# Optimization experiments

Hardware: AMD Instinct MI355X
Metric: run time of the kernel (lower is better)

## Reference

```python
import jax, jax.numpy as jnp
import numpy as np

F = 3          # features
E = 2 * F      # transformer d_model
H = F          # n_heads (head_dim = 2)
FF = 2048      # torch TransformerEncoderLayer default dim_feedforward
OUT = 4
STRIDE = 2
N_BATCH = 16
T_LEN = 2046
LN_EPS = 1e-5


def setup_inputs() -> dict:
    key = jax.random.key(0)
    ks = iter(jax.random.split(key, 48))

    def p(shape, s=0.1):
        return jax.random.normal(next(ks), shape, dtype=jnp.float32) * s

    inp = {
        "x": jax.random.normal(next(ks), (N_BATCH, T_LEN, F), dtype=jnp.float32),
        # multi-scale depthwise conv kernels/biases
        "k64": p((8, F, 64)), "b64": p((8, F)),
        "k16": p((F, 16)), "b16": p((F,)),
        "k8": p((F, 8)), "b8": p((F,)),
        # stage-2 width-3 channel convs
        "kw3": p((F, 3)), "bw3": p((F,)),
        "km3": p((F, 3)), "bm3": p((F,)),
        "kn3": p((F, 3)), "bn3": p((F,)),
        # hidden FCs
        "fc1_w": p((6 * F, 12 * F)), "fc1_b": p((6 * F,)),
        "fc2_w": p((E, 6 * F)), "fc2_b": p((E,)),
        # 2 transformer encoder layers (stacked along leading dim)
        "inw": p((2, 3 * E, E)), "inb": p((2, 3 * E)),
        "ow": p((2, E, E)), "ob": p((2, E)),
        "l1w": jnp.ones((2, E), jnp.float32), "l1b": jnp.zeros((2, E), jnp.float32),
        "l2w": jnp.ones((2, E), jnp.float32), "l2b": jnp.zeros((2, E), jnp.float32),
        "f1w": p((2, FF, E)), "f1b": p((2, FF)),
        "f2w": p((2, E, FF)), "f2b": p((2, E)),
        # output head
        "out1_w": p((7, E)), "out1_b": p((7,)),
        "out2_w": p((OUT, 7)),
    }
    return inp


def _ln(y, w, b):
    mu = y.mean(-1, keepdims=True)
    var = ((y - mu) ** 2).mean(-1, keepdims=True)
    return (y - mu) / jnp.sqrt(var + LN_EPS) * w + b


def _conv3_same(y, k, b):
    # depthwise width-3 'same' conv over seq dim; y:(N,L,F), k:(F,3), b:(F,)
    yp = jnp.pad(y, ((0, 0), (1, 1), (0, 0)))
    return k[:, 0] * yp[:, :-2] + k[:, 1] * yp[:, 1:-1] + k[:, 2] * yp[:, 2:] + b


def _forward(x, k64, b64, k16, b16, k8, b8, kw3, bw3, km3, bm3, kn3, bn3,
             fc1_w, fc1_b, fc2_w, fc2_b, inw, inb, ow, ob,
             l1w, l1b, l2w, l2b, f1w, f1b, f2w, f2b, out1_w, out1_b, out2_w):
    N, T, _ = x.shape
    PAD = 40
    px = jnp.pad(x, ((0, 0), (PAD, PAD), (0, 0)))
    W = T // STRIDE + 1
    centers = PAD + 1 + STRIDE * jnp.arange(W)  # wide window centers
    starts = centers - 32
    relu = jax.nn.relu

    # wide: 8 depthwise width-64 kernels per center -> (N, 8W, F)
    wwin = px[:, centers[:, None] + jnp.arange(-32, 32), :]        # (N,W,64,F)
    wide = jnp.einsum('nwtf,kft->nwkf', wwin, k64) + b64[None, None]
    wide = wide.reshape(N, 8 * W, F)  # center-major, kernel-minor (loop order)

    # mid: width-16 kernel at 8 centers per window -> (N, 8W, F)
    mid_c = (starts[:, None] + 8 * jnp.arange(8)).reshape(-1)
    mwin = px[:, mid_c[:, None] + jnp.arange(-8, 8), :]            # (N,8W,16,F)
    mid = jnp.einsum('nctf,ft->ncf', mwin, k16) + b16

    # narrow: width-8 kernel at 32 centers per window, then maxpool4 -> (N, 8W, F)
    nar_c = (starts[:, None] + 2 * jnp.arange(32)).reshape(-1)
    nwin = px[:, nar_c[:, None] + jnp.arange(-4, 4), :]            # (N,32W,8,F)
    nar = jnp.einsum('nctf,ft->ncf', nwin, k8) + b8
    nar = nar.reshape(N, 8 * W, 4, F).max(axis=2)

    wide = 5.0 * relu(wide)  # residual=0, dropout=0 -> drop is identity
    mid = relu(mid)
    nar = relu(nar)

    wide = relu(_conv3_same(wide, kw3, bw3))
    mid = relu(_conv3_same(mid, km3, bm3))
    nar = relu(_conv3_same(nar, kn3, bn3))

    def pool2(y):  # MaxPool1d(2) over seq dim
        return y.reshape(N, 4 * W, 2, F).max(axis=2)
    wide, mid, nar = pool2(wide), pool2(mid), pool2(nar)

    S = W  # (4W) // 4 blocks

    def blocks(y):  # (N,4W,F) -> (N,S,4F), time-major flatten per block
        return y.reshape(N, S, 4 * F)
    flat = jnp.concatenate([blocks(wide), blocks(mid), blocks(nar)], axis=-1)

    h = relu(flat @ fc1_w.T + fc1_b)  # residual=0 -> (1-residual)*h + 0
    h = relu(h @ fc2_w.T + fc2_b)     # (N,S,E)
    seq = jnp.transpose(h, (1, 0, 2))  # (S,N,E), torch seq-first layout

    d = E // H
    scale = 1.0 / jnp.sqrt(jnp.float32(d))
    for l in range(2):  # post-LN TransformerEncoder, 2 layers
        qkv = seq @ inw[l].T + inb[l]                 # (S,N,3E)
        q, k_, v = jnp.split(qkv, 3, axis=-1)
        q = q.reshape(S, N, H, d)
        k_ = k_.reshape(S, N, H, d)
        v = v.reshape(S, N, H, d)
        att = jnp.einsum('snhd,tnhd->nhst', q, k_) * scale
        p_att = jax.nn.softmax(att, axis=-1)
        o = jnp.einsum('nhst,tnhd->snhd', p_att, v).reshape(S, N, E)
        o = o @ ow[l].T + ob[l]
        seq = _ln(seq + o, l1w[l], l1b[l])
        ff = relu(seq @ f1w[l].T + f1b[l]) @ f2w[l].T + f2b[l]
        seq = _ln(seq + ff, l2w[l], l2b[l])

    pooled = relu(seq.mean(axis=0))           # AvgPool1d over full seq -> (N,E)
    o1 = relu(pooled @ out1_w.T + out1_b)
    logits = o1 @ out2_w.T                    # no bias
    return jax.nn.log_softmax(logits, axis=1)


def reference(x, k64, b64, k16, b16, k8, b8, kw3, bw3, km3, bm3, kn3, bn3,
              fc1_w, fc1_b, fc2_w, fc2_b, inw, inb, ow, ob,
              l1w, l1b, l2w, l2b, f1w, f1b, f2w, f2b, out1_w, out1_b, out2_w):
    return _forward(x, k64, b64, k16, b16, k8, b8, kw3, bw3, km3, bm3, kn3, bn3,
                    fc1_w, fc1_b, fc2_w, fc2_b, inw, inb, ow, ob,
                    l1w, l1b, l2w, l2b, f1w, f1b, f2w, f2b, out1_w, out1_b, out2_w)
```

## Files before the change

kernel.cpp:

```cpp
#include <hip/hip_runtime.h>
#include <math.h>


#define TL 2046
#define SL 1024

typedef float f32x2 __attribute__((ext_vector_type(2)));

__device__ __forceinline__ float relu_(float a){ return fmaxf(a, 0.f); }
__device__ __forceinline__ float fexp2_(float x){ return __builtin_amdgcn_exp2f(x); }
__device__ __forceinline__ float dpp_xadd1(float x){
  return x + __int_as_float(__builtin_amdgcn_update_dpp(
      0, __float_as_int(x), 0xB1, 0xF, 0xF, true));
}
__device__ __forceinline__ float dpp_xadd2(float x){
  return x + __int_as_float(__builtin_amdgcn_update_dpp(
      0, __float_as_int(x), 0x4E, 0xF, 0xF, true));
}

__device__ __forceinline__ f32x2 pk_fma_blo(f32x2 a, f32x2 b, f32x2 c){
  f32x2 d;
  asm("v_pk_fma_f32 %0, %1, %2, %3 op_sel:[0,0,0] op_sel_hi:[1,0,1]"
      : "=v"(d) : "v"(a), "v"(b), "v"(c));
  return d;
}
__device__ __forceinline__ f32x2 pk_fma_bhi(f32x2 a, f32x2 b, f32x2 c){
  f32x2 d;
  asm("v_pk_fma_f32 %0, %1, %2, %3 op_sel:[0,1,0] op_sel_hi:[1,1,1]"
      : "=v"(d) : "v"(a), "v"(b), "v"(c));
  return d;
}
__device__ __forceinline__ f32x2 pk_fma_blo_clo(f32x2 a, f32x2 b, f32x2 c){
  f32x2 d;
  asm("v_pk_fma_f32 %0, %1, %2, %3 op_sel:[0,0,0] op_sel_hi:[1,0,0]"
      : "=v"(d) : "v"(a), "v"(b), "v"(c));
  return d;
}
__device__ __forceinline__ f32x2 pk_mul_bhi(f32x2 a, f32x2 b){
  f32x2 d;
  asm("v_pk_mul_f32 %0, %1, %2 op_sel:[0,1] op_sel_hi:[1,1]"
      : "=v"(d) : "v"(a), "v"(b));
  return d;
}
__device__ __forceinline__ f32x2 pk_add2(f32x2 a, f32x2 b){
  f32x2 d;
  asm("v_pk_add_f32 %0, %1, %2" : "=v"(d) : "v"(a), "v"(b));
  return d;
}

#define SCQK 1.0201265650432017f

__global__ __launch_bounds__(192) void frontend_kernel(
  const float* __restrict__ x, const float* __restrict__ k64,
  const float* __restrict__ b64, const float* __restrict__ k16, const float* __restrict__ b16,
  const float* __restrict__ k8,  const float* __restrict__ b8,
  const float* __restrict__ kw3, const float* __restrict__ bw3,
  const float* __restrict__ km3, const float* __restrict__ bm3,
  const float* __restrict__ kn3, const float* __restrict__ bn3,
  const float* __restrict__ fc1w, const float* __restrict__ fc1b,
  const float* __restrict__ fc2w, const float* __restrict__ fc2b,
  const float* __restrict__ f1w, const float* __restrict__ f1b,
  const float* __restrict__ f2w,
  const float* __restrict__ inw, const float* __restrict__ inb,
  float* __restrict__ fcc, float* __restrict__ seq,
  float4* __restrict__ kv4, float2* __restrict__ qq)
{
  __shared__ float xt[3][200];
  __shared__ float k64s[3*64*8];
  __shared__ float flat_s[64][44];
  __shared__ float h1_s[64][20];
  __shared__ float seq6[64][6];
  const int tid  = threadIdx.x;
  const int f    = tid >> 6;
  const int lane = tid & 63;
  const int n    = blockIdx.x >> 4;
  const int s0   = (blockIdx.x & 15) << 6;
  const int s    = s0 + lane;

  for (int i = blockIdx.x*192 + tid; i < 2*2048*16; i += 256*192){
    int l = i >> 15, r = i & 32767, j = r >> 4, c = r & 15;
    float v = 0.f;
    if (c < 6)       v = f1w[(l*2048 + j)*6 + c];
    else if (c == 6) v = f1b[l*2048 + j];
    else if (c >= 8 && c < 14) v = f2w[(l*6 + (c-8))*2048 + j];
    fcc[i] = v;
  }

  for (int i = tid; i < 600; i += 192){
    int ff = i / 200, pos = i - ff*200;
    int xp = 2*s0 - 39 + pos;
    xt[ff][pos] = (xp >= 0 && xp < TL) ? x[(n*TL + xp)*3 + ff] : 0.f;
  }
  for (int i = tid; i < 1536; i += 192){
    int ff = i >> 9, r = i & 511, t = r >> 3, k = r & 7;
    k64s[i] = k64[k*192 + ff*64 + t];
  }
  __syncthreads();

  float xr[74];
  {
    const int b = 2*lane;
    #pragma unroll
    for (int i = 0; i < 74; i++) xr[i] = xt[f][b + i];
  }

  float accw[8], acc_e0, acc_e1;
  #pragma unroll
  for (int k = 0; k < 8; k++) accw[k] = b64[k*3 + f];
  acc_e0 = accw[7]; acc_e1 = accw[0];
  {
    const float* kp = &k64s[f*512];
    #pragma unroll
    for (int t = 0; t < 64; t++){
      float4 wa = *(const float4*)(kp + t*8);
      float4 wb = *(const float4*)(kp + t*8 + 4);
      float xm = xr[8 + t];
      accw[0] = fmaf(xm, wa.x, accw[0]);
      accw[1] = fmaf(xm, wa.y, accw[1]);
      accw[2] = fmaf(xm, wa.z, accw[2]);
      accw[3] = fmaf(xm, wa.w, accw[3]);
      accw[4] = fmaf(xm, wb.x, accw[4]);
      accw[5] = fmaf(xm, wb.y, accw[5]);
      accw[6] = fmaf(xm, wb.z, accw[6]);
      accw[7] = fmaf(xm, wb.w, accw[7]);
      acc_e0 = fmaf(xr[6 + t],  wb.w, acc_e0);
      acc_e1 = fmaf(xr[10 + t], wa.x, acc_e1);
    }
  }
  float yw[10];
  yw[0] = (s > 0) ? 5.f*relu_(acc_e0) : 0.f;
  #pragma unroll
  for (int c = 1; c <= 8; c++) yw[c] = 5.f*relu_(accw[c-1]);
  yw[9] = (s < 1023) ? 5.f*relu_(acc_e1) : 0.f;

  float w16r[16];
  #pragma unroll
  for (int t = 0; t < 16; t++) w16r[t] = k16[f*16 + t];
  const float bb16 = b16[f];
  float ym[10];
  #pragma unroll
  for (int ci = 0; ci < 10; ci++){
    const int b = (ci == 0) ? 54 : ((ci == 9) ? 2 : 8*(ci-1));
    float a = bb16;
    #pragma unroll
    for (int t = 0; t < 16; t++) a = fmaf(xr[b + t], w16r[t], a);
    ym[ci] = relu_(a);
  }
  if (s == 0)    ym[0] = 0.f;
  if (s == 1023) ym[9] = 0.f;

  float w8r[8];
  #pragma unroll
  for (int t = 0; t < 8; t++) w8r[t] = k8[f*8 + t];
  const float bb8 = b8[f];
  float yn[10];
  #pragma unroll
  for (int ci = 0; ci < 10; ci++){
    float m = -3.0e38f;
    #pragma unroll
    for (int j2 = 0; j2 < 4; j2++){
      const int b = (ci == 0) ? (58 + 2*j2)
                  : ((ci == 9) ? (6 + 2*j2)
                               : (4 + 2*(4*(ci-1) + j2)));
      float a = bb8;
      #pragma unroll
      for (int t = 0; t < 8; t++) a = fmaf(xr[b + t], w8r[t], a);
      m = fmaxf(m, a);
    }
    yn[ci] = relu_(m);
  }
  if (s == 0)    yn[0] = 0.f;
  if (s == 1023) yn[9] = 0.f;

  {
    float c0 = kw3[f*3], c1 = kw3[f*3+1], c2 = kw3[f*3+2], bb = bw3[f];
    #pragma unroll
    for (int q = 0; q < 4; q++){
      float z0 = relu_(fmaf(c0, yw[2*q],   fmaf(c1, yw[2*q+1], fmaf(c2, yw[2*q+2], bb))));
      float z1 = relu_(fmaf(c0, yw[2*q+1], fmaf(c1, yw[2*q+2], fmaf(c2, yw[2*q+3], bb))));
      flat_s[lane][q*3 + f] = fmaxf(z0, z1);
    }
  }
  {
    float c0 = km3[f*3], c1 = km3[f*3+1], c2 = km3[f*3+2], bb = bm3[f];
    #pragma unroll
    for (int q = 0; q < 4; q++){
      float z0 = relu_(fmaf(c0, ym[2*q],   fmaf(c1, ym[2*q+1], fmaf(c2, ym[2*q+2], bb))));
      float z1 = relu_(fmaf(c0, ym[2*q+1], fmaf(c1, ym[2*q+2], fmaf(c2, ym[2*q+3], bb))));
      flat_s[lane][12 + q*3 + f] = fmaxf(z0, z1);
    }
  }
  {
    float c0 = kn3[f*3], c1 = kn3[f*3+1], c2 = kn3[f*3+2], bb = bn3[f];
    #pragma unroll
    for (int q = 0; q < 4; q++){
      float z0 = relu_(fmaf(c0, yn[2*q],   fmaf(c1, yn[2*q+1], fmaf(c2, yn[2*q+2], bb))));
      float z1 = relu_(fmaf(c0, yn[2*q+1], fmaf(c1, yn[2*q+2], fmaf(c2, yn[2*q+3], bb))));
      flat_s[lane][24 + q*3 + f] = fmaxf(z0, z1);
    }
  }
  __syncthreads();

  #pragma unroll
  for (int oi = 0; oi < 6; oi++){
    const int o = 6*f + oi;
    float acc = fc1b[o];
    const float4* wrow = (const float4*)(fc1w + o*36);
    const float4* frow = (const float4*)(&flat_s[lane][0]);
    #pragma unroll
    for (int i = 0; i < 9; i++){
      float4 wv = wrow[i], fv = frow[i];
      acc = fmaf(wv.x, fv.x, acc); acc = fmaf(wv.y, fv.y, acc);
      acc = fmaf(wv.z, fv.z, acc); acc = fmaf(wv.w, fv.w, acc);
    }
    h1_s[lane][o] = relu_(acc);
  }
  __syncthreads();

  #pragma unroll
  for (int ei = 0; ei < 2; ei++){
    const int e = 2*f + ei;
    float acc = fc2b[e];
    #pragma unroll
    for (int o = 0; o < 18; o++) acc = fmaf(h1_s[lane][o], fc2w[e*18 + o], acc);
    float v = acc < 0.f ? 0.f : acc;
    seq[(n*SL + s)*6 + e] = v;
    seq6[lane][e] = v;
  }
  __syncthreads();

  {
    const int g = f;
    float sv[6];
    #pragma unroll
    for (int e = 0; e < 6; e++) sv[e] = seq6[lane][e];
    const int h2 = 2*g;
    float q0 = inb[h2],   q1 = inb[h2+1];
    float k0 = inb[6+h2], k1 = inb[7+h2];
    float v0 = inb[12+h2], v1 = inb[13+h2];
    #pragma unroll
    for (int e = 0; e < 6; e++){
      q0 = fmaf(sv[e], inw[h2*6 + e],      q0);
      q1 = fmaf(sv[e], inw[(h2+1)*6 + e],  q1);
      k0 = fmaf(sv[e], inw[(6+h2)*6 + e],  k0);
      k1 = fmaf(sv[e], inw[(7+h2)*6 + e],  k1);
      v0 = fmaf(sv[e], inw[(12+h2)*6 + e], v0);
      v1 = fmaf(sv[e], inw[(13+h2)*6 + e], v1);
    }
    const int nh = n*3 + g;
    kv4[nh*SL + s] = make_float4(k0*SCQK, k1*SCQK, v0, v1);
    qq [nh*SL + s] = make_float2(q0, q1);
  }
}

__global__ __launch_bounds__(512, 4) void attn_kernel(
  const float4* __restrict__ kv4, const float2* __restrict__ qq,
  float* __restrict__ att_out)
{
  __shared__ float4 sKV[1024];
  __shared__ float red[8][8][8][3];
  const int tid  = threadIdx.x;
  const int w    = tid >> 6;
  const int lane = tid & 63;
  const int rb   = blockIdx.x << 6;
  const int h    = blockIdx.y;
  const int n    = blockIdx.z;
  const int nh   = n*3 + h;

  const float4* kvp = kv4 + nh*SL;
  sKV[tid]       = kvp[tid];
  sKV[tid + 512] = kvp[tid + 512];

  const int r0 = rb + w*8;
  f32x2 q0p[4], q1p[4];
  {
    const float2* qp = qq + nh*SL + r0;
    #pragma unroll
    for (int p = 0; p < 4; p++){
      float2 qa = qp[2*p], qb = qp[2*p+1];
      q0p[p] = f32x2{qa.x, qb.x};
      q1p[p] = f32x2{qa.y, qb.y};
    }
  }
  __syncthreads();

  f32x2 lvp[4], o0p[4], o1p[4];
  #pragma unroll
  for (int p = 0; p < 4; p++){ lvp[p] = 0.f; o0p[p] = 0.f; o1p[p] = 0.f; }

  #pragma unroll 2
  for (int i = 0; i < 16; i++){
    float4 K = sKV[i*64 + lane];
    f32x2 pA = f32x2{K.x, K.y};
    f32x2 pB = f32x2{K.z, K.w};
    #pragma unroll
    for (int p = 0; p < 4; p++){
      f32x2 sc = pk_fma_blo(q0p[p], pA, pk_mul_bhi(q1p[p], pA));
      f32x2 pe;
      pe.x = fexp2_(sc.x);
      pe.y = fexp2_(sc.y);
      lvp[p] = pk_add2(lvp[p], pe);
      o0p[p] = pk_fma_blo(pe, pB, o0p[p]);
      o1p[p] = pk_fma_bhi(pe, pB, o1p[p]);
    }
  }

  float lv[8], o0[8], o1[8];
  #pragma unroll
  for (int p = 0; p < 4; p++){
    lv[2*p] = lvp[p].x;  lv[2*p+1] = lvp[p].y;
    o0[2*p] = o0p[p].x;  o0[2*p+1] = o0p[p].y;
    o1[2*p] = o1p[p].x;  o1[2*p+1] = o1p[p].y;
  }
  #pragma unroll
  for (int r = 0; r < 8; r++){
    lv[r] = dpp_xadd1(lv[r]); lv[r] = dpp_xadd2(lv[r]); lv[r] += __shfl_xor(lv[r], 4);
    o0[r] = dpp_xadd1(o0[r]); o0[r] = dpp_xadd2(o0[r]); o0[r] += __shfl_xor(o0[r], 4);
    o1[r] = dpp_xadd1(o1[r]); o1[r] = dpp_xadd2(o1[r]); o1[r] += __shfl_xor(o1[r], 4);
  }
  {
    const int g = lane >> 3;
    #pragma unroll
    for (int r = 0; r < 8; r++){
      if ((lane & 7) == r){
        red[w][g][r][0] = lv[r];
        red[w][g][r][1] = o0[r];
        red[w][g][r][2] = o1[r];
      }
    }
  }
  __syncthreads();

  if (tid < 64){
    const int ww = tid >> 3, r = tid & 7;
    float L = 0.f, O0 = 0.f, O1 = 0.f;
    #pragma unroll
    for (int g = 0; g < 8; g++){
      L  += red[ww][g][r][0];
      O0 += red[ww][g][r][1];
      O1 += red[ww][g][r][2];
    }
    const float inv = 1.0f / L;
    float* orow = att_out + (n*SL + rb + tid)*6 + 2*h;
    orow[0] = O0*inv; orow[1] = O1*inv;
  }
}

__global__ __launch_bounds__(512, 4) void ff_kernel(
  const float* __restrict__ seq_in, const float* __restrict__ att,
  const float* __restrict__ fcc,
  const float* __restrict__ ow, const float* __restrict__ ob,
  const float* __restrict__ l1w, const float* __restrict__ l1b,
  float* __restrict__ seq_mid, float* __restrict__ ffp, int layer)
{
  __shared__ float wc[512][16];
  __shared__ float sM[128][6];
  const int tid   = threadIdx.x;
  const int tile  = blockIdx.x >> 2;
  const int slice = blockIdx.x & 3;
  const int tok0  = tile * 128;

  const float4* FC = (const float4*)(fcc + (size_t)(layer*2048 + slice*512)*16);
  for (int i = tid; i < 2048; i += 512)
    ((float4*)wc)[i] = FC[i];

  if (tid < 128){
    const int token = tok0 + tid;
    const float* a  = att + token*6;
    const float* W  = ow + layer*36;
    float av[6];
    #pragma unroll
    for (int e = 0; e < 6; e++) av[e] = a[e];
    float y[6]; float mu = 0.f;
    #pragma unroll
    for (int e = 0; e < 6; e++){
      float o = ob[layer*6 + e];
      #pragma unroll
      for (int e2 = 0; e2 < 6; e2++) o = fmaf(av[e2], W[e*6 + e2], o);
      y[e] = seq_in[token*6 + e] + o;
      mu += y[e];
    }
    mu *= (1.f/6.f);
    float var = 0.f;
    #pragma unroll
    for (int e = 0; e < 6; e++){ float d = y[e] - mu; var = fmaf(d, d, var); }
    var *= (1.f/6.f);
    float rstd = rsqrtf(var + 1e-5f);
    #pragma unroll
    for (int e = 0; e < 6; e++)
      sM[tid][e] = (y[e] - mu)*rstd*l1w[layer*6 + e] + l1b[layer*6 + e];
  }
  __syncthreads();

  const int w = tid >> 6, lane = tid & 63, tp = lane >> 2, ss = lane & 3;

  f32x2 sv2[4][6];
  {
    const float* sp = &sM[tp*8][0];
    #pragma unroll
    for (int p = 0; p < 4; p++)
      #pragma unroll
      for (int e = 0; e < 6; e++)
        sv2[p][e] = f32x2{sp[(2*p)*6 + e], sp[(2*p+1)*6 + e]};
  }
  f32x2 acc2[4][6];
  #pragma unroll
  for (int p = 0; p < 4; p++)
    #pragma unroll
    for (int e = 0; e < 6; e++) acc2[p][e] = 0.f;

  const int rbase = w*64 + ss;
  #pragma unroll 2
  for (int i = 0; i < 16; i++){
    const f32x2* wr = (const f32x2*)&wc[rbase + i*4][0];
    f32x2 p0 = wr[0], p1 = wr[1], p2 = wr[2], p3 = wr[3];
    f32x2 p4 = wr[4], p5 = wr[5], p6 = wr[6];
    #pragma unroll
    for (int p = 0; p < 4; p++){
      f32x2 h = pk_fma_blo_clo(sv2[p][0], p0, p3);
      h = pk_fma_bhi(sv2[p][1], p0, h);
      h = pk_fma_blo(sv2[p][2], p1, h);
      h = pk_fma_bhi(sv2[p][3], p1, h);
      h = pk_fma_blo(sv2[p][4], p2, h);
      h = pk_fma_bhi(sv2[p][5], p2, h);
      h.x = fmaxf(h.x, 0.f);
      h.y = fmaxf(h.y, 0.f);
      acc2[p][0] = pk_fma_blo(h, p4, acc2[p][0]);
      acc2[p][1] = pk_fma_bhi(h, p4, acc2[p][1]);
      acc2[p][2] = pk_fma_blo(h, p5, acc2[p][2]);
      acc2[p][3] = pk_fma_bhi(h, p5, acc2[p][3]);
      acc2[p][4] = pk_fma_blo(h, p6, acc2[p][4]);
      acc2[p][5] = pk_fma_bhi(h, p6, acc2[p][5]);
    }
  }

  float acc[8][6];
  #pragma unroll
  for (int p = 0; p < 4; p++)
    #pragma unroll
    for (int e = 0; e < 6; e++){
      acc[2*p][e]   = acc2[p][e].x;
      acc[2*p+1][e] = acc2[p][e].y;
    }

  #pragma unroll
  for (int t = 0; t < 8; t++)
    #pragma unroll
    for (int e = 0; e < 6; e++){
      acc[t][e] = dpp_xadd1(acc[t][e]);
      acc[t][e] = dpp_xadd2(acc[t][e]);
    }
  __syncthreads();
  float* red = (float*)wc;
  if (ss == 0){
    #pragma unroll
    for (int t = 0; t < 8; t++)
      #pragma unroll
      for (int e = 0; e < 6; e++) red[(w*16 + tp)*48 + t*6 + e] = acc[t][e];
  }
  __syncthreads();
  for (int i = tid; i < 768; i += 512){
    const int tl = i / 6, e = i - tl*6;
    const int rtp = tl >> 3, rt = tl & 7;
    float sum = 0.f;
    #pragma unroll
    for (int wv = 0; wv < 8; wv++)
      sum += red[(wv*16 + rtp)*48 + rt*6 + e];
    ffp[(size_t)(slice*16384 + tok0 + tl)*6 + e] = sum;
  }
  if (slice == 0 && tid < 128){
    #pragma unroll
    for (int e = 0; e < 6; e++) seq_mid[(tok0 + tid)*6 + e] = sM[tid][e];
  }
}

__global__ __launch_bounds__(128) void ffln_kernel(
  const float* __restrict__ seq_mid, const float* __restrict__ ffp,
  const float* __restrict__ f2b, const float* __restrict__ lw,
  const float* __restrict__ lb,
  const float* __restrict__ Wq, const float* __restrict__ Bq,
  float* __restrict__ seq_out, float4* __restrict__ kv4, float2* __restrict__ qq)
{
  const int tok = blockIdx.x*128 + threadIdx.x;
  float y[6]; float mu = 0.f;
  #pragma unroll
  for (int e = 0; e < 6; e++){
    float v = seq_mid[tok*6 + e] + f2b[e];
    v += ffp[(size_t)(0*16384 + tok)*6 + e];
    v += ffp[(size_t)(1*16384 + tok)*6 + e];
    v += ffp[(size_t)(2*16384 + tok)*6 + e];
    v += ffp[(size_t)(3*16384 + tok)*6 + e];
    y[e] = v; mu += v;
  }
  mu *= (1.f/6.f);
  float var = 0.f;
  #pragma unroll
  for (int e = 0; e < 6; e++){ float d = y[e] - mu; var = fmaf(d, d, var); }
  var *= (1.f/6.f);
  float rstd = rsqrtf(var + 1e-5f);
  float sv[6];
  #pragma unroll
  for (int e = 0; e < 6; e++){
    sv[e] = (y[e] - mu)*rstd*lw[e] + lb[e];
    seq_out[tok*6 + e] = sv[e];
  }

  const int n = tok >> 10, t = tok & 1023;
  #pragma unroll
  for (int g = 0; g < 3; g++){
    const int h2 = 2*g;
    float q0 = Bq[h2],   q1 = Bq[h2+1];
    float k0 = Bq[6+h2], k1 = Bq[7+h2];
    float v0 = Bq[12+h2], v1 = Bq[13+h2];
    #pragma unroll
    for (int e = 0; e < 6; e++){
      q0 = fmaf(sv[e], Wq[h2*6 + e],      q0);
      q1 = fmaf(sv[e], Wq[(h2+1)*6 + e],  q1);
      k0 = fmaf(sv[e], Wq[(6+h2)*6 + e],  k0);
      k1 = fmaf(sv[e], Wq[(7+h2)*6 + e],  k1);
      v0 = fmaf(sv[e], Wq[(12+h2)*6 + e], v0);
      v1 = fmaf(sv[e], Wq[(13+h2)*6 + e], v1);
    }
    const int nh = n*3 + g;
    kv4[nh*SL + t] = make_float4(k0*SCQK, k1*SCQK, v0, v1);
    qq [nh*SL + t] = make_float2(q0, q1);
  }
}

__global__ __launch_bounds__(256) void final_kernel(
  const float* __restrict__ seq_mid, const float* __restrict__ ffp,
  const float* __restrict__ f2b, const float* __restrict__ lw,
  const float* __restrict__ lb,
  const float* __restrict__ o1w, const float* __restrict__ o1b,
  const float* __restrict__ o2w, float* __restrict__ out)
{
  __shared__ float fred[4][6];
  __shared__ float pooled[6];
  const int n = blockIdx.x, tid = threadIdx.x;
  float psum[6] = {0,0,0,0,0,0};

  #pragma unroll
  for (int i = 0; i < 4; i++){
    const int tok = n*SL + tid + i*256;
    float y[6]; float mu = 0.f;
    #pragma unroll
    for (int e = 0; e < 6; e++){
      float v = seq_mid[tok*6 + e] + f2b[e];
      v += ffp[(size_t)(0*16384 + tok)*6 + e];
      v += ffp[(size_t)(1*16384 + tok)*6 + e];
      v += ffp[(size_t)(2*16384 + tok)*6 + e];
      v += ffp[(size_t)(3*16384 + tok)*6 + e];
      y[e] = v; mu += v;
    }
    mu *= (1.f/6.f);
    float var = 0.f;
    #pragma unroll
    for (int e = 0; e < 6; e++){ float d = y[e] - mu; var = fmaf(d, d, var); }
    var *= (1.f/6.f);
    float rstd = rsqrtf(var + 1e-5f);
    #pragma unroll
    for (int e = 0; e < 6; e++)
      psum[e] += (y[e] - mu)*rstd*lw[e] + lb[e];
  }

  #pragma unroll
  for (int e = 0; e < 6; e++){
    psum[e] += __shfl_xor(psum[e], 1);  psum[e] += __shfl_xor(psum[e], 2);
    psum[e] += __shfl_xor(psum[e], 4);  psum[e] += __shfl_xor(psum[e], 8);
    psum[e] += __shfl_xor(psum[e], 16); psum[e] += __shfl_xor(psum[e], 32);
  }
  if ((tid & 63) == 0){
    #pragma unroll
    for (int e = 0; e < 6; e++) fred[tid >> 6][e] = psum[e];
  }
  __syncthreads();
  if (tid < 6){
    float t = fred[0][tid] + fred[1][tid] + fred[2][tid] + fred[3][tid];
    pooled[tid] = fmaxf(t * (1.f/1024.f), 0.f);
  }
  __syncthreads();
  if (tid == 0){
    float o1[7];
    #pragma unroll
    for (int o = 0; o < 7; o++){
      float a = o1b[o];
      #pragma unroll
      for (int e2 = 0; e2 < 6; e2++) a = fmaf(pooled[e2], o1w[o*6 + e2], a);
      o1[o] = relu_(a);
    }
    float lg[4];
    #pragma unroll
    for (int c = 0; c < 4; c++){
      float a = 0.f;
      #pragma unroll
      for (int o = 0; o < 7; o++) a = fmaf(o1[o], o2w[c*7 + o], a);
      lg[c] = a;
    }
    float m = fmaxf(fmaxf(lg[0], lg[1]), fmaxf(lg[2], lg[3]));
    float sum = 0.f;
    #pragma unroll
    for (int c = 0; c < 4; c++) sum += expf(lg[c] - m);
    float lse = m + logf(sum);
    #pragma unroll
    for (int c = 0; c < 4; c++) out[n*4 + c] = lg[c] - lse;
  }
}

extern "C" void kernel_launch(void* const* d_in, const int* in_sizes, int n_in,
                              void* d_out, int out_size, void* d_ws, size_t ws_size,
                              hipStream_t stream)
{
  const float* x    = (const float*)d_in[0];
  const float* k64  = (const float*)d_in[1];
  const float* b64  = (const float*)d_in[2];
  const float* k16  = (const float*)d_in[3];
  const float* b16  = (const float*)d_in[4];
  const float* k8   = (const float*)d_in[5];
  const float* b8   = (const float*)d_in[6];
  const float* kw3  = (const float*)d_in[7];
  const float* bw3  = (const float*)d_in[8];
  const float* km3  = (const float*)d_in[9];
  const float* bm3  = (const float*)d_in[10];
  const float* kn3  = (const float*)d_in[11];
  const float* bn3  = (const float*)d_in[12];
  const float* fc1w = (const float*)d_in[13];
  const float* fc1b = (const float*)d_in[14];
  const float* fc2w = (const float*)d_in[15];
  const float* fc2b = (const float*)d_in[16];
  const float* inw  = (const float*)d_in[17];
  const float* inb  = (const float*)d_in[18];
  const float* ow   = (const float*)d_in[19];
  const float* ob   = (const float*)d_in[20];
  const float* l1w  = (const float*)d_in[21];
  const float* l1b  = (const float*)d_in[22];
  const float* l2w  = (const float*)d_in[23];
  const float* l2b  = (const float*)d_in[24];
  const float* f1w  = (const float*)d_in[25];
  const float* f1b  = (const float*)d_in[26];
  const float* f2w  = (const float*)d_in[27];
  const float* f2b  = (const float*)d_in[28];
  const float* o1w  = (const float*)d_in[29];
  const float* o1b  = (const float*)d_in[30];
  const float* o2w  = (const float*)d_in[31];
  float* out = (float*)d_out;

  float* w = (float*)d_ws;
  float*  seq_a   = w;
  float*  seq_b   = w + 98304;
  float*  att     = w + 196608;
  float*  seq_mid = w + 294912;
  float*  ffp     = w + 393216;
  float*  fcc     = w + 786432;
  float4* kv4     = (float4*)(w + 851968);
  float2* qq      = (float2*)(w + 1048576);

  frontend_kernel<<<256, 192, 0, stream>>>(x, k64, b64, k16, b16, k8, b8,
      kw3, bw3, km3, bm3, kn3, bn3, fc1w, fc1b, fc2w, fc2b,
      f1w, f1b, f2w, inw, inb, fcc, seq_a, kv4, qq);

  dim3 agrid(16, 3, 16);
  attn_kernel<<<agrid, 512, 0, stream>>>(kv4, qq, att);
  ff_kernel<<<512, 512, 0, stream>>>(seq_a, att, fcc, ow, ob, l1w, l1b,
      seq_mid, ffp, 0);
  ffln_kernel<<<128, 128, 0, stream>>>(seq_mid, ffp, f2b, l2w, l2b,
      inw + 108, inb + 18, seq_b, kv4, qq);

  attn_kernel<<<agrid, 512, 0, stream>>>(kv4, qq, att);
  ff_kernel<<<512, 512, 0, stream>>>(seq_b, att, fcc, ow, ob, l1w, l1b,
      seq_mid, ffp, 1);
  final_kernel<<<16, 256, 0, stream>>>(seq_mid, ffp, f2b + 6, l2w + 6, l2b + 6,
      o1w, o1b, o2w, out);
}
```

Baseline: 74.61 us.

## Offload weight repack to extra warp, retile FF kernel with swizzled LDS

The frontend kernel gains a fourth wavefront that handles the FF weight repack (fcc) while the other three load inputs and compute, so the repack overlaps instead of running serially. In ff_kernel each lane now handles 16 tokens and 8 weight rows instead of 8 tokens and 16 rows, which raises register reuse of the loaded weights. The reduction gains a cross-lane shuffle, and the weight tile in LDS is stored with a rotated 16-byte column swizzle to avoid bank conflicts. The occupancy hint is lowered to 2 to make room for the larger register footprint, at the cost of fewer waves in flight.

```diff
diff --git a/kernel.cpp b/kernel.cpp
--- a/kernel.cpp
+++ b/kernel.cpp
@@ -50,7 +50,7 @@
 
 #define SCQK 1.0201265650432017f
 
-__global__ __launch_bounds__(192) void frontend_kernel(
+__global__ __launch_bounds__(256) void frontend_kernel(
   const float* __restrict__ x, const float* __restrict__ k64,
   const float* __restrict__ b64, const float* __restrict__ k16, const float* __restrict__ b16,
   const float* __restrict__ k8,  const float* __restrict__ b8,
@@ -71,165 +71,176 @@
   __shared__ float h1_s[64][20];
   __shared__ float seq6[64][6];
   const int tid  = threadIdx.x;
-  const int f    = tid >> 6;
+  const int f    = (tid >> 6) & 3;
   const int lane = tid & 63;
   const int n    = blockIdx.x >> 4;
   const int s0   = (blockIdx.x & 15) << 6;
   const int s    = s0 + lane;
 
-  for (int i = blockIdx.x*192 + tid; i < 2*2048*16; i += 256*192){
-    int l = i >> 15, r = i & 32767, j = r >> 4, c = r & 15;
-    float v = 0.f;
-    if (c < 6)       v = f1w[(l*2048 + j)*6 + c];
-    else if (c == 6) v = f1b[l*2048 + j];
-    else if (c >= 8 && c < 14) v = f2w[(l*6 + (c-8))*2048 + j];
-    fcc[i] = v;
-  }
-
-  for (int i = tid; i < 600; i += 192){
-    int ff = i / 200, pos = i - ff*200;
-    int xp = 2*s0 - 39 + pos;
-    xt[ff][pos] = (xp >= 0 && xp < TL) ? x[(n*TL + xp)*3 + ff] : 0.f;
-  }
-  for (int i = tid; i < 1536; i += 192){
-    int ff = i >> 9, r = i & 511, t = r >> 3, k = r & 7;
-    k64s[i] = k64[k*192 + ff*64 + t];
-  }
-  __syncthreads();
-
-  float xr[74];
-  {
-    const int b = 2*lane;
-    #pragma unroll
-    for (int i = 0; i < 74; i++) xr[i] = xt[f][b + i];
-  }
-
-  float accw[8], acc_e0, acc_e1;
-  #pragma unroll
-  for (int k = 0; k < 8; k++) accw[k] = b64[k*3 + f];
-  acc_e0 = accw[7]; acc_e1 = accw[0];
-  {
-    const float* kp = &k64s[f*512];
-    #pragma unroll
-    for (int t = 0; t < 64; t++){
-      float4 wa = *(const float4*)(kp + t*8);
-      float4 wb = *(const float4*)(kp + t*8 + 4);
-      float xm = xr[8 + t];
-      accw[0] = fmaf(xm, wa.x, accw[0]);
-      accw[1] = fmaf(xm, wa.y, accw[1]);
-      accw[2] = fmaf(xm, wa.z, accw[2]);
-      accw[3] = fmaf(xm, wa.w, accw[3]);
-      accw[4] = fmaf(xm, wb.x, accw[4]);
-      accw[5] = fmaf(xm, wb.y, accw[5]);
-      accw[6] = fmaf(xm, wb.z, accw[6]);
-      accw[7] = fmaf(xm, wb.w, accw[7]);
-      acc_e0 = fmaf(xr[6 + t],  wb.w, acc_e0);
-      acc_e1 = fmaf(xr[10 + t], wa.x, acc_e1);
-    }
-  }
-  float yw[10];
-  yw[0] = (s > 0) ? 5.f*relu_(acc_e0) : 0.f;
-  #pragma unroll
-  for (int c = 1; c <= 8; c++) yw[c] = 5.f*relu_(accw[c-1]);
-  yw[9] = (s < 1023) ? 5.f*relu_(acc_e1) : 0.f;
-
-  float w16r[16];
-  #pragma unroll
-  for (int t = 0; t < 16; t++) w16r[t] = k16[f*16 + t];
-  const float bb16 = b16[f];
-  float ym[10];
-  #pragma unroll
-  for (int ci = 0; ci < 10; ci++){
-    const int b = (ci == 0) ? 54 : ((ci == 9) ? 2 : 8*(ci-1));
-    float a = bb16;
-    #pragma unroll
-    for (int t = 0; t < 16; t++) a = fmaf(xr[b + t], w16r[t], a);
-    ym[ci] = relu_(a);
-  }
-  if (s == 0)    ym[0] = 0.f;
-  if (s == 1023) ym[9] = 0.f;
-
-  float w8r[8];
-  #pragma unroll
-  for (int t = 0; t < 8; t++) w8r[t] = k8[f*8 + t];
-  const float bb8 = b8[f];
-  float yn[10];
-  #pragma unroll
-  for (int ci = 0; ci < 10; ci++){
-    float m = -3.0e38f;
-    #pragma unroll
-    for (int j2 = 0; j2 < 4; j2++){
-      const int b = (ci == 0) ? (58 + 2*j2)
-                  : ((ci == 9) ? (6 + 2*j2)
-                               : (4 + 2*(4*(ci-1) + j2)));
-      float a = bb8;
-      #pragma unroll
-      for (int t = 0; t < 8; t++) a = fmaf(xr[b + t], w8r[t], a);
-      m = fmaxf(m, a);
-    }
-    yn[ci] = relu_(m);
-  }
-  if (s == 0)    yn[0] = 0.f;
-  if (s == 1023) yn[9] = 0.f;
-
-  {
-    float c0 = kw3[f*3], c1 = kw3[f*3+1], c2 = kw3[f*3+2], bb = bw3[f];
-    #pragma unroll
-    for (int q = 0; q < 4; q++){
-      float z0 = relu_(fmaf(c0, yw[2*q],   fmaf(c1, yw[2*q+1], fmaf(c2, yw[2*q+2], bb))));
-      float z1 = relu_(fmaf(c0, yw[2*q+1], fmaf(c1, yw[2*q+2], fmaf(c2, yw[2*q+3], bb))));
-      flat_s[lane][q*3 + f] = fmaxf(z0, z1);
-    }
-  }
-  {
-    float c0 = km3[f*3], c1 = km3[f*3+1], c2 = km3[f*3+2], bb = bm3[f];
-    #pragma unroll
-    for (int q = 0; q < 4; q++){
-      float z0 = relu_(fmaf(c0, ym[2*q],   fmaf(c1, ym[2*q+1], fmaf(c2, ym[2*q+2], bb))));
-      float z1 = relu_(fmaf(c0, ym[2*q+1], fmaf(c1, ym[2*q+2], fmaf(c2, ym[2*q+3], bb))));
-      flat_s[lane][12 + q*3 + f] = fmaxf(z0, z1);
-    }
-  }
-  {
-    float c0 = kn3[f*3], c1 = kn3[f*3+1], c2 = kn3[f*3+2], bb = bn3[f];
-    #pragma unroll
-    for (int q = 0; q < 4; q++){
-      float z0 = relu_(fmaf(c0, yn[2*q],   fmaf(c1, yn[2*q+1], fmaf(c2, yn[2*q+2], bb))));
-      float z1 = relu_(fmaf(c0, yn[2*q+1], fmaf(c1, yn[2*q+2], fmaf(c2, yn[2*q+3], bb))));
-      flat_s[lane][24 + q*3 + f] = fmaxf(z0, z1);
-    }
-  }
-  __syncthreads();
-
-  #pragma unroll
-  for (int oi = 0; oi < 6; oi++){
-    const int o = 6*f + oi;
-    float acc = fc1b[o];
-    const float4* wrow = (const float4*)(fc1w + o*36);
-    const float4* frow = (const float4*)(&flat_s[lane][0]);
-    #pragma unroll
-    for (int i = 0; i < 9; i++){
-      float4 wv = wrow[i], fv = frow[i];
-      acc = fmaf(wv.x, fv.x, acc); acc = fmaf(wv.y, fv.y, acc);
-      acc = fmaf(wv.z, fv.z, acc); acc = fmaf(wv.w, fv.w, acc);
-    }
-    h1_s[lane][o] = relu_(acc);
-  }
-  __syncthreads();
-
-  #pragma unroll
-  for (int ei = 0; ei < 2; ei++){
-    const int e = 2*f + ei;
-    float acc = fc2b[e];
-    #pragma unroll
-    for (int o = 0; o < 18; o++) acc = fmaf(h1_s[lane][o], fc2w[e*18 + o], acc);
-    float v = acc < 0.f ? 0.f : acc;
-    seq[(n*SL + s)*6 + e] = v;
-    seq6[lane][e] = v;
-  }
-  __syncthreads();
-
-  {
+  if (tid >= 192){
+    const int base = (blockIdx.x*64 + (tid - 192))*4;
+    #pragma unroll
+    for (int k = 0; k < 4; k++){
+      const int i = base + k;
+      const int l = i >> 15, r = i & 32767, j = r >> 4, c = r & 15;
+      float v = 0.f;
+      if (c < 6)       v = f1w[(l*2048 + j)*6 + c];
+      else if (c == 6) v = f1b[l*2048 + j];
+      else if (c >= 8 && c < 14) v = f2w[(l*6 + (c-8))*2048 + j];
+      fcc[i] = v;
+    }
+  } else {
+    for (int i = tid; i < 600; i += 192){
+      int ff = i / 200, pos = i - ff*200;
+      int xp = 2*s0 - 39 + pos;
+      xt[ff][pos] = (xp >= 0 && xp < TL) ? x[(n*TL + xp)*3 + ff] : 0.f;
+    }
+    for (int i = tid; i < 1536; i += 192){
+      int ff = i >> 9, r = i & 511, t = r >> 3, k = r & 7;
+      k64s[i] = k64[k*192 + ff*64 + t];
+    }
+  }
+  __syncthreads();
+
+  if (tid < 192){
+    float xr[74];
+    {
+      const int b = 2*lane;
+      #pragma unroll
+      for (int i = 0; i < 74; i++) xr[i] = xt[f][b + i];
+    }
+
+    float accw[8], acc_e0, acc_e1;
+    #pragma unroll
+    for (int k = 0; k < 8; k++) accw[k] = b64[k*3 + f];
+    acc_e0 = accw[7]; acc_e1 = accw[0];
+    {
+      const float* kp = &k64s[f*512];
+      #pragma unroll
+      for (int t = 0; t < 64; t++){
+        float4 wa = *(const float4*)(kp + t*8);
+        float4 wb = *(const float4*)(kp + t*8 + 4);
+        float xm = xr[8 + t];
+        accw[0] = fmaf(xm, wa.x, accw[0]);
+        accw[1] = fmaf(xm, wa.y, accw[1]);
+        accw[2] = fmaf(xm, wa.z, accw[2]);
+        accw[3] = fmaf(xm, wa.w, accw[3]);
+        accw[4] = fmaf(xm, wb.x, accw[4]);
+        accw[5] = fmaf(xm, wb.y, accw[5]);
+        accw[6] = fmaf(xm, wb.z, accw[6]);
+        accw[7] = fmaf(xm, wb.w, accw[7]);
+        acc_e0 = fmaf(xr[6 + t],  wb.w, acc_e0);
+        acc_e1 = fmaf(xr[10 + t], wa.x, acc_e1);
+      }
+    }
+    float yw[10];
+    yw[0] = (s > 0) ? 5.f*relu_(acc_e0) : 0.f;
+    #pragma unroll
+    for (int c = 1; c <= 8; c++) yw[c] = 5.f*relu_(accw[c-1]);
+    yw[9] = (s < 1023) ? 5.f*relu_(acc_e1) : 0.f;
+
+    float w16r[16];
+    #pragma unroll
+    for (int t = 0; t < 16; t++) w16r[t] = k16[f*16 + t];
+    const float bb16 = b16[f];
+    float ym[10];
+    #pragma unroll
+    for (int ci = 0; ci < 10; ci++){
+      const int b = (ci == 0) ? 54 : ((ci == 9) ? 2 : 8*(ci-1));
+      float a = bb16;
+      #pragma unroll
+      for (int t = 0; t < 16; t++) a = fmaf(xr[b + t], w16r[t], a);
+      ym[ci] = relu_(a);
+    }
+    if (s == 0)    ym[0] = 0.f;
+    if (s == 1023) ym[9] = 0.f;
+
+    float w8r[8];
+    #pragma unroll
+    for (int t = 0; t < 8; t++) w8r[t] = k8[f*8 + t];
+    const float bb8 = b8[f];
+    float yn[10];
+    #pragma unroll
+    for (int ci = 0; ci < 10; ci++){
+      float m = -3.0e38f;
+      #pragma unroll
+      for (int j2 = 0; j2 < 4; j2++){
+        const int b = (ci == 0) ? (58 + 2*j2)
+                    : ((ci == 9) ? (6 + 2*j2)
+                                 : (4 + 2*(4*(ci-1) + j2)));
+        float a = bb8;
+        #pragma unroll
+        for (int t = 0; t < 8; t++) a = fmaf(xr[b + t], w8r[t], a);
+        m = fmaxf(m, a);
+      }
+      yn[ci] = relu_(m);
+    }
+    if (s == 0)    yn[0] = 0.f;
+    if (s == 1023) yn[9] = 0.f;
+
+    {
+      float c0 = kw3[f*3], c1 = kw3[f*3+1], c2 = kw3[f*3+2], bb = bw3[f];
+      #pragma unroll
+      for (int q = 0; q < 4; q++){
+        float z0 = relu_(fmaf(c0, yw[2*q],   fmaf(c1, yw[2*q+1], fmaf(c2, yw[2*q+2], bb))));
+        float z1 = relu_(fmaf(c0, yw[2*q+1], fmaf(c1, yw[2*q+2], fmaf(c2, yw[2*q+3], bb))));
+        flat_s[lane][q*3 + f] = fmaxf(z0, z1);
+      }
+    }
+    {
+      float c0 = km3[f*3], c1 = km3[f*3+1], c2 = km3[f*3+2], bb = bm3[f];
+      #pragma unroll
+      for (int q = 0; q < 4; q++){
+        float z0 = relu_(fmaf(c0, ym[2*q],   fmaf(c1, ym[2*q+1], fmaf(c2, ym[2*q+2], bb))));
+        float z1 = relu_(fmaf(c0, ym[2*q+1], fmaf(c1, ym[2*q+2], fmaf(c2, ym[2*q+3], bb))));
+        flat_s[lane][12 + q*3 + f] = fmaxf(z0, z1);
+      }
+    }
+    {
+      float c0 = kn3[f*3], c1 = kn3[f*3+1], c2 = kn3[f*3+2], bb = bn3[f];
+      #pragma unroll
+      for (int q = 0; q < 4; q++){
+        float z0 = relu_(fmaf(c0, yn[2*q],   fmaf(c1, yn[2*q+1], fmaf(c2, yn[2*q+2], bb))));
+        float z1 = relu_(fmaf(c0, yn[2*q+1], fmaf(c1, yn[2*q+2], fmaf(c2, yn[2*q+3], bb))));
+        flat_s[lane][24 + q*3 + f] = fmaxf(z0, z1);
+      }
+    }
+  }
+  __syncthreads();
+
+  if (tid < 192){
+    #pragma unroll
+    for (int oi = 0; oi < 6; oi++){
+      const int o = 6*f + oi;
+      float acc = fc1b[o];
+      const float4* wrow = (const float4*)(fc1w + o*36);
+      const float4* frow = (const float4*)(&flat_s[lane][0]);
+      #pragma unroll
+      for (int i = 0; i < 9; i++){
+        float4 wv = wrow[i], fv = frow[i];
+        acc = fmaf(wv.x, fv.x, acc); acc = fmaf(wv.y, fv.y, acc);
+        acc = fmaf(wv.z, fv.z, acc); acc = fmaf(wv.w, fv.w, acc);
+      }
+      h1_s[lane][o] = relu_(acc);
+    }
+  }
+  __syncthreads();
+
+  if (tid < 192){
+    #pragma unroll
+    for (int ei = 0; ei < 2; ei++){
+      const int e = 2*f + ei;
+      float acc = fc2b[e];
+      #pragma unroll
+      for (int o = 0; o < 18; o++) acc = fmaf(h1_s[lane][o], fc2w[e*18 + o], acc);
+      float v = acc < 0.f ? 0.f : acc;
+      seq[(n*SL + s)*6 + e] = v;
+      seq6[lane][e] = v;
+    }
+  }
+  __syncthreads();
+
+  if (tid < 192){
     const int g = f;
     float sv[6];
     #pragma unroll
@@ -346,7 +357,7 @@
   }
 }
 
-__global__ __launch_bounds__(512, 4) void ff_kernel(
+__global__ __launch_bounds__(512, 2) void ff_kernel(
   const float* __restrict__ seq_in, const float* __restrict__ att,
   const float* __restrict__ fcc,
   const float* __restrict__ ow, const float* __restrict__ ob,
@@ -361,8 +372,10 @@
   const int tok0  = tile * 128;
 
   const float4* FC = (const float4*)(fcc + (size_t)(layer*2048 + slice*512)*16);
-  for (int i = tid; i < 2048; i += 512)
-    ((float4*)wc)[i] = FC[i];
+  for (int i = tid; i < 2048; i += 512){
+    const int row = i >> 2, wd = i & 3;
+    ((float4*)wc)[(row << 2) + ((wd + (row >> 1)) & 3)] = FC[i];
+  }
 
   if (tid < 128){
     const int token = tok0 + tid;
@@ -392,31 +405,38 @@
   }
   __syncthreads();
 
-  const int w = tid >> 6, lane = tid & 63, tp = lane >> 2, ss = lane & 3;
-
-  f32x2 sv2[4][6];
+  const int w = tid >> 6, lane = tid & 63, tp = lane >> 3, ss = lane & 7;
+
+  f32x2 sv2[8][6];
   {
-    const float* sp = &sM[tp*8][0];
-    #pragma unroll
-    for (int p = 0; p < 4; p++)
+    const float* sp = &sM[tp*16][0];
+    #pragma unroll
+    for (int p = 0; p < 8; p++)
       #pragma unroll
       for (int e = 0; e < 6; e++)
         sv2[p][e] = f32x2{sp[(2*p)*6 + e], sp[(2*p+1)*6 + e]};
   }
-  f32x2 acc2[4][6];
-  #pragma unroll
-  for (int p = 0; p < 4; p++)
+  f32x2 acc2[8][6];
+  #pragma unroll
+  for (int p = 0; p < 8; p++)
     #pragma unroll
     for (int e = 0; e < 6; e++) acc2[p][e] = 0.f;
 
-  const int rbase = w*64 + ss;
   #pragma unroll 2
-  for (int i = 0; i < 16; i++){
-    const f32x2* wr = (const f32x2*)&wc[rbase + i*4][0];
-    f32x2 p0 = wr[0], p1 = wr[1], p2 = wr[2], p3 = wr[3];
-    f32x2 p4 = wr[4], p5 = wr[5], p6 = wr[6];
-    #pragma unroll
-    for (int p = 0; p < 4; p++){
+  for (int i = 0; i < 8; i++){
+    const int r = (w << 6) + ss + (i << 3);
+    const int rot = (r >> 1) & 3;
+    const float* rowp = &wc[r][0];
+    const f32x2* rw0 = (const f32x2*)(rowp + ((((0 + rot) & 3)) << 2));
+    const f32x2* rw1 = (const f32x2*)(rowp + ((((1 + rot) & 3)) << 2));
+    const f32x2* rw2 = (const f32x2*)(rowp + ((((2 + rot) & 3)) << 2));
+    const f32x2* rw3 = (const f32x2*)(rowp + ((((3 + rot) & 3)) << 2));
+    f32x2 p0 = rw0[0], p1 = rw0[1];
+    f32x2 p2 = rw1[0], p3 = rw1[1];
+    f32x2 p4 = rw2[0], p5 = rw2[1];
+    f32x2 p6 = rw3[0];
+    #pragma unroll
+    for (int p = 0; p < 8; p++){
       f32x2 h = pk_fma_blo_clo(sv2[p][0], p0, p3);
       h = pk_fma_bhi(sv2[p][1], p0, h);
       h = pk_fma_blo(sv2[p][2], p1, h);
@@ -434,9 +454,9 @@
     }
   }
 
-  float acc[8][6];
-  #pragma unroll
-  for (int p = 0; p < 4; p++)
+  float acc[16][6];
+  #pragma unroll
+  for (int p = 0; p < 8; p++)
     #pragma unroll
     for (int e = 0; e < 6; e++){
       acc[2*p][e]   = acc2[p][e].x;
@@ -444,28 +464,29 @@
     }
 
   #pragma unroll
-  for (int t = 0; t < 8; t++)
+  for (int t = 0; t < 16; t++)
     #pragma unroll
     for (int e = 0; e < 6; e++){
       acc[t][e] = dpp_xadd1(acc[t][e]);
       acc[t][e] = dpp_xadd2(acc[t][e]);
+      acc[t][e] += __shfl_xor(acc[t][e], 4);
     }
   __syncthreads();
   float* red = (float*)wc;
   if (ss == 0){
     #pragma unroll
-    for (int t = 0; t < 8; t++)
-      #pragma unroll
-      for (int e = 0; e < 6; e++) red[(w*16 + tp)*48 + t*6 + e] = acc[t][e];
+    for (int t = 0; t < 16; t++)
+      #pragma unroll
+      for (int e = 0; e < 6; e++) red[(w*8 + tp)*96 + t*6 + e] = acc[t][e];
   }
   __syncthreads();
   for (int i = tid; i < 768; i += 512){
     const int tl = i / 6, e = i - tl*6;
-    const int rtp = tl >> 3, rt = tl & 7;
+    const int rtp = tl >> 4, rt = tl & 15;
     float sum = 0.f;
     #pragma unroll
     for (int wv = 0; wv < 8; wv++)
-      sum += red[(wv*16 + rtp)*48 + rt*6 + e];
+      sum += red[(wv*8 + rtp)*96 + rt*6 + e];
     ffp[(size_t)(slice*16384 + tok0 + tl)*6 + e] = sum;
   }
   if (slice == 0 && tid < 128){
@@ -654,7 +675,7 @@
   float4* kv4     = (float4*)(w + 851968);
   float2* qq      = (float2*)(w + 1048576);
 
-  frontend_kernel<<<256, 192, 0, stream>>>(x, k64, b64, k16, b16, k8, b8,
+  frontend_kernel<<<256, 256, 0, stream>>>(x, k64, b64, k16, b16, k8, b8,
       kw3, bw3, km3, bm3, kn3, bn3, fc1w, fc1b, fc2w, fc2b,
       f1w, f1b, f2w, inw, inb, fcc, seq_a, kv4, qq);
 
```

Result: slower. 94.72 us (+27.0%).
